# Kernel optimization log

Measured on AMD Instinct MI355X. Metric: run time of the kernel, lower is better.

The kernel has to match this reference:

```python
import jax, jax.numpy as jnp
import numpy as np

HIDDEN = 1024
NUM_HEADS = 16
HEAD_DIM = HIDDEN // NUM_HEADS  # 64
B, S = 2, 2048


def setup_inputs() -> dict:
    key = jax.random.key(0)
    ks = jax.random.split(key, 10)
    sd = 1.0 / np.sqrt(HIDDEN)
    x = jax.random.normal(ks[0], (B, S, HIDDEN), dtype=jnp.float32)
    # per-head projections stacked over head axis: [H, hidden, head_dim]
    Wq = jax.random.normal(ks[1], (NUM_HEADS, HIDDEN, HEAD_DIM), dtype=jnp.float32) * sd
    Wk = jax.random.normal(ks[2], (NUM_HEADS, HIDDEN, HEAD_DIM), dtype=jnp.float32) * sd
    Wv = jax.random.normal(ks[3], (NUM_HEADS, HIDDEN, HEAD_DIM), dtype=jnp.float32) * sd
    bq = jax.random.normal(ks[4], (NUM_HEADS, HEAD_DIM), dtype=jnp.float32) * sd
    bk = jax.random.normal(ks[5], (NUM_HEADS, HEAD_DIM), dtype=jnp.float32) * sd
    bv = jax.random.normal(ks[6], (NUM_HEADS, HEAD_DIM), dtype=jnp.float32) * sd
    # output projection: [all_head_size, hidden]
    Wo = jax.random.normal(ks[7], (HIDDEN, HIDDEN), dtype=jnp.float32) * sd
    bo = jax.random.normal(ks[8], (HIDDEN,), dtype=jnp.float32) * sd
    return {"x": x, "Wq": Wq, "bq": bq, "Wk": Wk, "bk": bk,
            "Wv": Wv, "bv": bv, "Wo": Wo, "bo": bo}


def reference(x, Wq, bq, Wk, bk, Wv, bv, Wo, bo):
    # Fused-across-heads equivalent of the per-head Python loop.
    # q,k,v: [B, H, S, Dh]
    q = jnp.einsum('bsd,hde->bhse', x, Wq) + bq[None, :, None, :]
    k = jnp.einsum('bsd,hde->bhse', x, Wk) + bk[None, :, None, :]
    v = jnp.einsum('bsd,hde->bhse', x, Wv) + bv[None, :, None, :]
    scale = 1.0 / jnp.sqrt(jnp.asarray(HEAD_DIM, dtype=x.dtype))
    scores = jnp.einsum('bhse,bhte->bhst', q, k) * scale  # [B,H,S,S]
    probs = jax.nn.softmax(scores, axis=-1)               # dropout=0 (eval)
    ctx = jnp.einsum('bhst,bhte->bhse', probs, v)         # [B,H,S,Dh]
    # concat heads on last dim (head order matches torch.cat over heads)
    ctx = jnp.transpose(ctx, (0, 2, 1, 3)).reshape(x.shape[0], x.shape[1], -1)
    out = ctx @ Wo + bo                                   # output projection
    return out
```

## Files before the change

kernel.cpp:

```cpp
#include <hip/hip_runtime.h>
#include <cstdint>

typedef unsigned short u16;
typedef __attribute__((ext_vector_type(8))) short short8;
typedef __attribute__((ext_vector_type(4))) short short4v;
typedef __attribute__((ext_vector_type(4))) float f32x4;
typedef __attribute__((ext_vector_type(4))) unsigned short u16x4;

__device__ __forceinline__ u16 f2bf(float x) {
    unsigned int u = __float_as_uint(x);
    u += 0x7fffu + ((u >> 16) & 1u);
    return (u16)(u >> 16);
}

__device__ __forceinline__ float fexp2(float x) {
#if __has_builtin(__builtin_amdgcn_exp2f)
    return __builtin_amdgcn_exp2f(x);
#else
    return exp2f(x);
#endif
}

__device__ __forceinline__ unsigned pack_bf16(float a, float b) {
    unsigned ua = __float_as_uint(a) + 0x8000u;
    unsigned ub = __float_as_uint(b) + 0x8000u;
    return __builtin_amdgcn_perm(ub, ua, 0x07060302u);
}

#if __has_builtin(__builtin_amdgcn_mfma_f32_16x16x16bf16_1k)
__device__ __forceinline__ f32x4 mfma16(short4v a, short4v b, f32x4 c) {
    return __builtin_amdgcn_mfma_f32_16x16x16bf16_1k(a, b, c, 0, 0, 0);
}
#else
__device__ __forceinline__ f32x4 mfma16(short4v a, short4v b, f32x4 c) {
    short8 a8 = {a[0], a[1], a[2], a[3], 0, 0, 0, 0};
    short8 b8 = {b[0], b[1], b[2], b[3], 0, 0, 0, 0};
    return __builtin_amdgcn_mfma_f32_16x16x32_bf16(a8, b8, c, 0, 0, 0);
}
#endif

__device__ __forceinline__ void gload_lds16(const u16* g, u16* l) {
    __builtin_amdgcn_global_load_lds(
        (const __attribute__((address_space(1))) void*)(g),
        (__attribute__((address_space(3))) void*)(l),
        16, 0, 0);
}

__global__ __launch_bounds__(256) void prep_kernel(
    const float* __restrict__ x,
    const float* __restrict__ Wq, const float* __restrict__ Wk,
    const float* __restrict__ Wv, const float* __restrict__ Wo,
    u16* __restrict__ xb, u16* __restrict__ wqkv, u16* __restrict__ wot)
{
    __shared__ u16 tile[64][65];
    const int z = blockIdx.z;
    const int tc = threadIdx.x & 63, tr = threadIdx.x >> 6;

    if (z == 1) {
        const int blk = blockIdx.y * 16 + blockIdx.x;
        const int base = (blk * 256 + threadIdx.x) * 4;
        #pragma unroll
        for (int i = 0; i < 16; ++i) {
            const int idx = base + i * 262144;
            float4 v = *(const float4*)(x + idx);
            u16x4 o;
            o.x = f2bf(v.x); o.y = f2bf(v.y); o.z = f2bf(v.z); o.w = f2bf(v.w);
            *(u16x4*)(xb + idx) = o;
        }
        return;
    }

    const float* src;
    u16* dst;
    int C, R, rb, cb;
    if (z == 0) {
        src = Wo; dst = wot; C = 1024; R = 1024;
        rb = blockIdx.x * 64; cb = blockIdx.y * 64;
    } else {
        const float* W = (z == 2) ? Wq : (z == 3) ? Wk : Wv;
        const int head = blockIdx.y;
        src = W + head * 65536;
        dst = wqkv + (size_t)(z - 2) * 1048576 + head * 65536;
        C = 64; R = 1024;
        rb = blockIdx.x * 64; cb = 0;
    }
    #pragma unroll
    for (int i = 0; i < 64; i += 4)
        tile[tr + i][tc] = f2bf(src[(size_t)(rb + tr + i) * C + (cb + tc)]);
    __syncthreads();
    #pragma unroll
    for (int i = 0; i < 64; i += 4)
        dst[(size_t)(cb + tr + i) * R + (rb + tc)] = tile[tc][tr + i];
}

__global__ __launch_bounds__(256, 3) void gemm_qkv_kernel(
    const u16* __restrict__ X, const u16* __restrict__ W,
    const float* __restrict__ bq, const float* __restrict__ bk,
    const float* __restrict__ bv,
    u16* __restrict__ qo, u16* __restrict__ ko, u16* __restrict__ vto)
{
    __shared__ __align__(16) u16 As[128 * 32];
    __shared__ __align__(16) u16 Bs[128 * 32];
    const int tid = threadIdx.x;
    const int lane = tid & 63;
    const int wv = tid >> 6;
    const int wm = wv & 1, wn = wv >> 1;
    const int m0 = blockIdx.y * 128;
    const int n0 = blockIdx.x * 128;
    const int c = lane & 15, qd = lane >> 4;

    f32x4 acc[4][4];
    #pragma unroll
    for (int a = 0; a < 4; ++a)
        #pragma unroll
        for (int b2 = 0; b2 < 4; ++b2) acc[a][b2] = f32x4{0.f, 0.f, 0.f, 0.f};

    const u16* Xb = X + (size_t)m0 * 1024;
    const u16* Wb = W + (size_t)n0 * 1024;

    for (int kt = 0; kt < 1024; kt += 32) {
        #pragma unroll
        for (int i = 0; i < 2; ++i) {
            int slot = i * 256 + tid;
            int row = slot >> 2, part = slot & 3;
            gload_lds16(Xb + (size_t)row * 1024 + kt + part * 8, &As[slot * 8]);
            gload_lds16(Wb + (size_t)row * 1024 + kt + part * 8, &Bs[slot * 8]);
        }
        __syncthreads();
        short8 af[4], bf[4];
        #pragma unroll
        for (int mt = 0; mt < 4; ++mt)
            af[mt] = *(const short8*)&As[(wm * 64 + mt * 16 + c) * 32 + qd * 8];
        #pragma unroll
        for (int nt = 0; nt < 4; ++nt)
            bf[nt] = *(const short8*)&Bs[(wn * 64 + nt * 16 + c) * 32 + qd * 8];
        #pragma unroll
        for (int mt = 0; mt < 4; ++mt)
            #pragma unroll
            for (int nt = 0; nt < 4; ++nt)
                acc[mt][nt] = __builtin_amdgcn_mfma_f32_16x16x32_bf16(af[mt], bf[nt], acc[mt][nt], 0, 0, 0);
        __syncthreads();
    }

    #pragma unroll
    for (int mt = 0; mt < 4; ++mt) {
        const int mbase = m0 + wm * 64 + mt * 16 + qd * 4;
        const int b = mbase >> 11;
        #pragma unroll
        for (int nt = 0; nt < 4; ++nt) {
            const int n = n0 + wn * 64 + nt * 16 + c;
            const int mat = n >> 10;
            const int idx = n & 1023;
            const int h = idx >> 6, e = idx & 63;
            const float bias = (mat == 0 ? bq : (mat == 1 ? bk : bv))[idx];
            if (mat == 2) {
                const int s = mbase & 2047;
                u16x4 pv;
                pv.x = f2bf(acc[mt][nt][0] + bias);
                pv.y = f2bf(acc[mt][nt][1] + bias);
                pv.z = f2bf(acc[mt][nt][2] + bias);
                pv.w = f2bf(acc[mt][nt][3] + bias);
                *(u16x4*)(vto + ((((size_t)(b * 16 + h) * 128 + (s >> 4)) * 64 + e) * 16
                                 + (s & 15))) = pv;
            } else {
                const float scale = (mat == 0) ? 0.18033688011112042f : 1.0f;
                u16* dst = (mat == 0) ? qo : ko;
                #pragma unroll
                for (int r = 0; r < 4; ++r) {
                    const int s = (mbase + r) & 2047;
                    dst[((size_t)((b * 16 + h) * 2048 + s)) * 64 + e] =
                        f2bf((acc[mt][nt][r] + bias) * scale);
                }
            }
        }
    }
}

__global__ __launch_bounds__(256, 3) void flash_kernel(
    const u16* __restrict__ Q,
    const u16* __restrict__ K,
    const u16* __restrict__ V2,
    u16* __restrict__ ctx)
{
    __shared__ __align__(16) char pool[34816];
    u16* stage = (u16*)pool;
    float (*Os)[64][66] = (float (*)[64][66])pool;
    float (*Ls)[64] = (float (*)[64])(pool + 33792);

    const int tid = threadIdx.x, lane = tid & 63, w = tid >> 6;
    const int c = lane & 15, qd = lane >> 4;
    const int bid = blockIdx.x;
    const int r5 = bid & 31;
    const int bh = (r5 & 7) * 4 + (r5 >> 3);
    const int q0 = (bid >> 5) * 64;
    const int b = bh >> 4, h = bh & 15;
    const u16* Qh = Q + (size_t)bh * 2048 * 64;
    const u16* Kh = K + (size_t)bh * 2048 * 64;
    const u16* Vh = V2 + (size_t)bh * 128 * 1024;

    u16* Kst = stage + w * 3072;

    const int krow8 = lane >> 3;
    const int kgc = (lane & 7) ^ (krow8 & 7);
    const int voff = c * 16 + qd * 4;

    short8 qf[4][2];
    #pragma unroll
    for (int qb = 0; qb < 4; ++qb)
        #pragma unroll
        for (int kb = 0; kb < 2; ++kb)
            qf[qb][kb] = *(const short8*)&Qh[(size_t)(q0 + qb * 16 + c) * 64 + kb * 32 + qd * 8];

    f32x4 o[4][4];
    float lsum[4];
    #pragma unroll
    for (int mt = 0; mt < 4; ++mt)
        #pragma unroll
        for (int qb = 0; qb < 4; ++qb) o[mt][qb] = f32x4{0.f, 0.f, 0.f, 0.f};
    #pragma unroll
    for (int qb = 0; qb < 4; ++qb) lsum[qb] = 0.f;

    #pragma unroll
    for (int j = 0; j < 2; ++j) {
        const int row = j * 8 + krow8;
        gload_lds16(Kh + (size_t)(w * 512 + row) * 64 + kgc * 8,
                    Kst + j * 512 + lane * 8);
    }
    short4v vA[4], vB[4];
    {
        const u16* vb = Vh + (size_t)(w * 32) * 1024 + voff;
        #pragma unroll
        for (int mt = 0; mt < 4; ++mt)
            vA[mt] = *(const short4v*)(vb + mt * 256);
    }
    #pragma unroll
    for (int j = 0; j < 2; ++j) {
        const int row = j * 8 + krow8;
        gload_lds16(Kh + (size_t)(w * 512 + 16 + row) * 64 + kgc * 8,
                    Kst + 1024 + j * 512 + lane * 8);
    }

    int cur = 0;
    auto body = [&](int it, short4v (&VC)[4], short4v (&VN)[4]) {
        u16* Kb = Kst + cur * 1024;

        __builtin_amdgcn_s_waitcnt(0xF74);
        __builtin_amdgcn_sched_barrier(0);

        short8 kf[2];
        #pragma unroll
        for (int kb = 0; kb < 2; ++kb)
            kf[kb] = *(const short8*)&Kb[c * 64 + ((4 * kb + qd) ^ (c & 7)) * 8];

        __builtin_amdgcn_sched_barrier(0);

        {
            const int itn = (it + 1) & 31;
            const u16* vb = Vh + (size_t)(w * 32 + itn) * 1024 + voff;
            #pragma unroll
            for (int mt = 0; mt < 4; ++mt)
                VN[mt] = *(const short4v*)(vb + mt * 256);
        }
        {
            const int itn = (it + 2) & 31;
            const int t0n = w * 512 + itn * 16;
            const int nslot = (cur >= 1) ? cur - 1 : 2;
            u16* Kn = Kst + nslot * 1024;
            #pragma unroll
            for (int j = 0; j < 2; ++j) {
                const int row = j * 8 + krow8;
                gload_lds16(Kh + (size_t)(t0n + row) * 64 + kgc * 8,
                            Kn + j * 512 + lane * 8);
            }
        }

        f32x4 sc[4];
        #pragma unroll
        for (int qb = 0; qb < 4; ++qb) {
            sc[qb] = f32x4{0.f, 0.f, 0.f, 0.f};
            sc[qb] = __builtin_amdgcn_mfma_f32_16x16x32_bf16(kf[0], qf[qb][0], sc[qb], 0, 0, 0);
            sc[qb] = __builtin_amdgcn_mfma_f32_16x16x32_bf16(kf[1], qf[qb][1], sc[qb], 0, 0, 0);
        }

        short4v pb[4];
        #pragma unroll
        for (int qb = 0; qb < 4; ++qb) {
            float p0 = fexp2(sc[qb][0]);
            float p1 = fexp2(sc[qb][1]);
            float p2 = fexp2(sc[qb][2]);
            float p3 = fexp2(sc[qb][3]);
            lsum[qb] += (p0 + p1) + (p2 + p3);
            unsigned d0 = pack_bf16(p0, p1);
            unsigned d1 = pack_bf16(p2, p3);
            union { unsigned u[2]; short4v s; } pu;
            pu.u[0] = d0; pu.u[1] = d1;
            pb[qb] = pu.s;
        }

        #pragma unroll
        for (int qb = 0; qb < 4; ++qb)
            #pragma unroll
            for (int mt = 0; mt < 4; ++mt)
                o[mt][qb] = mfma16(VC[mt], pb[qb], o[mt][qb]);

        cur = (cur == 2) ? 0 : cur + 1;
    };

    for (int it2 = 0; it2 < 16; ++it2) {
        body(2 * it2, vA, vB);
        body(2 * it2 + 1, vB, vA);
    }

    __builtin_amdgcn_s_waitcnt(0xF70);
    __syncthreads();

    #pragma unroll
    for (int qb = 0; qb < 4; ++qb) {
        lsum[qb] += __shfl_xor(lsum[qb], 16, 64);
        lsum[qb] += __shfl_xor(lsum[qb], 32, 64);
    }
    if (qd == 0) {
        #pragma unroll
        for (int qb = 0; qb < 4; ++qb) Ls[w][qb * 16 + c] = lsum[qb];
    }

    if (w >= 2) {
        float (*S)[66] = Os[w - 2];
        #pragma unroll
        for (int mt = 0; mt < 4; ++mt)
            #pragma unroll
            for (int qb = 0; qb < 4; ++qb)
                #pragma unroll
                for (int r = 0; r < 4; ++r)
                    S[mt * 16 + qd * 4 + r][qb * 16 + c] = o[mt][qb][r];
    }
    __syncthreads();
    if (w < 2) {
        float (*S)[66] = Os[w];
        #pragma unroll
        for (int mt = 0; mt < 4; ++mt)
            #pragma unroll
            for (int qb = 0; qb < 4; ++qb)
                #pragma unroll
                for (int r = 0; r < 4; ++r)
                    o[mt][qb][r] += S[mt * 16 + qd * 4 + r][qb * 16 + c];
    }
    __syncthreads();
    if (w == 1) {
        float (*S)[66] = Os[0];
        #pragma unroll
        for (int mt = 0; mt < 4; ++mt)
            #pragma unroll
            for (int qb = 0; qb < 4; ++qb)
                #pragma unroll
                for (int r = 0; r < 4; ++r)
                    S[mt * 16 + qd * 4 + r][qb * 16 + c] = o[mt][qb][r];
    }
    __syncthreads();
    if (w == 0) {
        float (*S)[66] = Os[0];
        float inv[4];
        #pragma unroll
        for (int qb = 0; qb < 4; ++qb) {
            int q = qb * 16 + c;
            float l = (Ls[0][q] + Ls[1][q]) + (Ls[2][q] + Ls[3][q]);
            inv[qb] = __builtin_amdgcn_rcpf(l);
        }
        #pragma unroll
        for (int mt = 0; mt < 4; ++mt)
            #pragma unroll
            for (int qb = 0; qb < 4; ++qb) {
                u16x4 ov;
                #pragma unroll
                for (int r = 0; r < 4; ++r) {
                    float v = (o[mt][qb][r] + S[mt * 16 + qd * 4 + r][qb * 16 + c]) * inv[qb];
                    ((u16*)&ov)[r] = f2bf(v);
                }
                *(u16x4*)&ctx[((size_t)(b * 2048 + q0 + qb * 16 + c)) * 1024
                              + h * 64 + mt * 16 + qd * 4] = ov;
            }
    }
}

__global__ __launch_bounds__(256, 4) void gemm_out_kernel(
    const u16* __restrict__ A, const u16* __restrict__ Wt,
    const float* __restrict__ bo, float* __restrict__ out)
{
    __shared__ __align__(16) u16 As[64 * 32];
    __shared__ __align__(16) u16 Bs[128 * 32];
    const int tid = threadIdx.x;
    const int lane = tid & 63;
    const int wv = tid >> 6;
    const int wm = wv & 1, wn = wv >> 1;
    const int m0 = blockIdx.x * 64;
    const int n0 = blockIdx.y * 128;
    const int c = lane & 15, qd = lane >> 4;

    f32x4 acc[2][4];
    #pragma unroll
    for (int a = 0; a < 2; ++a)
        #pragma unroll
        for (int b2 = 0; b2 < 4; ++b2) acc[a][b2] = f32x4{0.f, 0.f, 0.f, 0.f};

    const u16* Ab = A + (size_t)m0 * 1024;
    const u16* Wb = Wt + (size_t)n0 * 1024;

    for (int kt = 0; kt < 1024; kt += 32) {
        {
            int row = tid >> 2, part = tid & 3;
            gload_lds16(Ab + (size_t)row * 1024 + kt + part * 8, &As[tid * 8]);
        }
        #pragma unroll
        for (int i = 0; i < 2; ++i) {
            int slot = i * 256 + tid;
            int row = slot >> 2, part = slot & 3;
            gload_lds16(Wb + (size_t)row * 1024 + kt + part * 8, &Bs[slot * 8]);
        }
        __syncthreads();
        short8 af[2], bf[4];
        #pragma unroll
        for (int mt = 0; mt < 2; ++mt)
            af[mt] = *(const short8*)&As[(wm * 32 + mt * 16 + c) * 32 + qd * 8];
        #pragma unroll
        for (int nt = 0; nt < 4; ++nt)
            bf[nt] = *(const short8*)&Bs[(wn * 64 + nt * 16 + c) * 32 + qd * 8];
        #pragma unroll
        for (int mt = 0; mt < 2; ++mt)
            #pragma unroll
            for (int nt = 0; nt < 4; ++nt)
                acc[mt][nt] = __builtin_amdgcn_mfma_f32_16x16x32_bf16(af[mt], bf[nt], acc[mt][nt], 0, 0, 0);
        __syncthreads();
    }

    #pragma unroll
    for (int mt = 0; mt < 2; ++mt) {
        const int mbase = m0 + wm * 32 + mt * 16 + qd * 4;
        #pragma unroll
        for (int nt = 0; nt < 4; ++nt) {
            const int n = n0 + wn * 64 + nt * 16 + c;
            const float bias = bo[n];
            #pragma unroll
            for (int r = 0; r < 4; ++r)
                out[(size_t)(mbase + r) * 1024 + n] = acc[mt][nt][r] + bias;
        }
    }
}

extern "C" void kernel_launch(void* const* d_in, const int* in_sizes, int n_in,
                              void* d_out, int out_size, void* d_ws, size_t ws_size,
                              hipStream_t stream) {
    const float* x  = (const float*)d_in[0];
    const float* Wq = (const float*)d_in[1];
    const float* bq = (const float*)d_in[2];
    const float* Wk = (const float*)d_in[3];
    const float* bk = (const float*)d_in[4];
    const float* Wv = (const float*)d_in[5];
    const float* bv = (const float*)d_in[6];
    const float* Wo = (const float*)d_in[7];
    const float* bo = (const float*)d_in[8];
    float* out = (float*)d_out;

    u16* ws    = (u16*)d_ws;
    u16* xb    = ws;
    u16* wqkv  = xb + 4096 * 1024;
    u16* wot   = wqkv + 3072 * 1024;
    u16* qws   = wot + 1024 * 1024;
    u16* kws   = qws + 4194304;
    u16* v2ws  = kws + 4194304;
    u16* ctxws = v2ws + 4194304;

    prep_kernel<<<dim3(16, 16, 5), 256, 0, stream>>>(x, Wq, Wk, Wv, Wo, xb, wqkv, wot);
    gemm_qkv_kernel<<<dim3(24, 32), 256, 0, stream>>>(xb, wqkv, bq, bk, bv, qws, kws, v2ws);
    flash_kernel<<<1024, 256, 0, stream>>>(qws, kws, v2ws, ctxws);
    gemm_out_kernel<<<dim3(64, 8), 256, 0, stream>>>(ctxws, wot, bo, out);
}
```

Measured before the change: 190.7 us.

## Make flash attention kernel persistent with atomic work-queue tile scheduling

Converts the flash attention kernel into a persistent kernel launched with 768 blocks, each pulling (batch-head, query-tile) work items from a global atomic counter until all 1024 tiles are done. The goal is to cut tail imbalance and block launch overhead when the tile count is not a multiple of the resident block count. It also changes the tile ordering from the previous interleaved bh mapping to a contiguous one, which can affect L2 reuse of K/V. It adds a memset, an atomic and an extra sync per tile, and it falls back to the old launch when the workspace is too small to hold the counter.

```diff
diff --git a/kernel.cpp b/kernel.cpp
--- a/kernel.cpp
+++ b/kernel.cpp
@@ -180,23 +180,17 @@
     const u16* __restrict__ Q,
     const u16* __restrict__ K,
     const u16* __restrict__ V2,
-    u16* __restrict__ ctx)
+    u16* __restrict__ ctx,
+    unsigned* tcnt)
 {
     __shared__ __align__(16) char pool[34816];
+    __shared__ unsigned sh_t;
     u16* stage = (u16*)pool;
     float (*Os)[64][66] = (float (*)[64][66])pool;
     float (*Ls)[64] = (float (*)[64])(pool + 33792);
 
     const int tid = threadIdx.x, lane = tid & 63, w = tid >> 6;
     const int c = lane & 15, qd = lane >> 4;
-    const int bid = blockIdx.x;
-    const int r5 = bid & 31;
-    const int bh = (r5 & 7) * 4 + (r5 >> 3);
-    const int q0 = (bid >> 5) * 64;
-    const int b = bh >> 4, h = bh & 15;
-    const u16* Qh = Q + (size_t)bh * 2048 * 64;
-    const u16* Kh = K + (size_t)bh * 2048 * 64;
-    const u16* Vh = V2 + (size_t)bh * 128 * 1024;
 
     u16* Kst = stage + w * 3072;
 
@@ -204,181 +198,199 @@
     const int kgc = (lane & 7) ^ (krow8 & 7);
     const int voff = c * 16 + qd * 4;
 
-    short8 qf[4][2];
-    #pragma unroll
-    for (int qb = 0; qb < 4; ++qb)
-        #pragma unroll
-        for (int kb = 0; kb < 2; ++kb)
-            qf[qb][kb] = *(const short8*)&Qh[(size_t)(q0 + qb * 16 + c) * 64 + kb * 32 + qd * 8];
-
-    f32x4 o[4][4];
-    float lsum[4];
-    #pragma unroll
-    for (int mt = 0; mt < 4; ++mt)
-        #pragma unroll
-        for (int qb = 0; qb < 4; ++qb) o[mt][qb] = f32x4{0.f, 0.f, 0.f, 0.f};
-    #pragma unroll
-    for (int qb = 0; qb < 4; ++qb) lsum[qb] = 0.f;
-
-    #pragma unroll
-    for (int j = 0; j < 2; ++j) {
-        const int row = j * 8 + krow8;
-        gload_lds16(Kh + (size_t)(w * 512 + row) * 64 + kgc * 8,
-                    Kst + j * 512 + lane * 8);
-    }
-    short4v vA[4], vB[4];
-    {
-        const u16* vb = Vh + (size_t)(w * 32) * 1024 + voff;
+    for (;;) {
+        if (tid == 0)
+            sh_t = tcnt ? atomicAdd(tcnt, 1u) : (unsigned)blockIdx.x;
+        __syncthreads();
+        const unsigned t = sh_t;
+        if (t >= 1024u) break;
+
+        const int bh = (int)(t >> 5);
+        const int q0 = (int)(t & 31) << 6;
+        const int b = bh >> 4, h = bh & 15;
+        const u16* Qh = Q + (size_t)bh * 131072;
+        const u16* Kh = K + (size_t)bh * 131072;
+        const u16* Vh = V2 + (size_t)bh * 131072;
+
+        short8 qf[4][2];
+        #pragma unroll
+        for (int qb = 0; qb < 4; ++qb)
+            #pragma unroll
+            for (int kb = 0; kb < 2; ++kb)
+                qf[qb][kb] = *(const short8*)&Qh[(size_t)(q0 + qb * 16 + c) * 64 + kb * 32 + qd * 8];
+
+        f32x4 o[4][4];
+        float lsum[4];
         #pragma unroll
         for (int mt = 0; mt < 4; ++mt)
-            vA[mt] = *(const short4v*)(vb + mt * 256);
-    }
-    #pragma unroll
-    for (int j = 0; j < 2; ++j) {
-        const int row = j * 8 + krow8;
-        gload_lds16(Kh + (size_t)(w * 512 + 16 + row) * 64 + kgc * 8,
-                    Kst + 1024 + j * 512 + lane * 8);
-    }
-
-    int cur = 0;
-    auto body = [&](int it, short4v (&VC)[4], short4v (&VN)[4]) {
-        u16* Kb = Kst + cur * 1024;
-
-        __builtin_amdgcn_s_waitcnt(0xF74);
-        __builtin_amdgcn_sched_barrier(0);
-
-        short8 kf[2];
-        #pragma unroll
-        for (int kb = 0; kb < 2; ++kb)
-            kf[kb] = *(const short8*)&Kb[c * 64 + ((4 * kb + qd) ^ (c & 7)) * 8];
-
-        __builtin_amdgcn_sched_barrier(0);
-
+            #pragma unroll
+            for (int qb = 0; qb < 4; ++qb) o[mt][qb] = f32x4{0.f, 0.f, 0.f, 0.f};
+        #pragma unroll
+        for (int qb = 0; qb < 4; ++qb) lsum[qb] = 0.f;
+
+        #pragma unroll
+        for (int j = 0; j < 2; ++j) {
+            const int row = j * 8 + krow8;
+            gload_lds16(Kh + (size_t)(w * 512 + row) * 64 + kgc * 8,
+                        Kst + j * 512 + lane * 8);
+        }
+        short4v vA[4], vB[4];
         {
-            const int itn = (it + 1) & 31;
-            const u16* vb = Vh + (size_t)(w * 32 + itn) * 1024 + voff;
+            const u16* vb = Vh + (size_t)(w * 32) * 1024 + voff;
             #pragma unroll
             for (int mt = 0; mt < 4; ++mt)
-                VN[mt] = *(const short4v*)(vb + mt * 256);
-        }
-        {
-            const int itn = (it + 2) & 31;
-            const int t0n = w * 512 + itn * 16;
-            const int nslot = (cur >= 1) ? cur - 1 : 2;
-            u16* Kn = Kst + nslot * 1024;
-            #pragma unroll
-            for (int j = 0; j < 2; ++j) {
-                const int row = j * 8 + krow8;
-                gload_lds16(Kh + (size_t)(t0n + row) * 64 + kgc * 8,
-                            Kn + j * 512 + lane * 8);
-            }
-        }
-
-        f32x4 sc[4];
+                vA[mt] = *(const short4v*)(vb + mt * 256);
+        }
+        #pragma unroll
+        for (int j = 0; j < 2; ++j) {
+            const int row = j * 8 + krow8;
+            gload_lds16(Kh + (size_t)(w * 512 + 16 + row) * 64 + kgc * 8,
+                        Kst + 1024 + j * 512 + lane * 8);
+        }
+
+        int cur = 0;
+        auto body = [&](int it, short4v (&VC)[4], short4v (&VN)[4]) {
+            u16* Kb = Kst + cur * 1024;
+
+            __builtin_amdgcn_s_waitcnt(0xF74);
+            __builtin_amdgcn_sched_barrier(0);
+
+            short8 kf[2];
+            #pragma unroll
+            for (int kb = 0; kb < 2; ++kb)
+                kf[kb] = *(const short8*)&Kb[c * 64 + ((4 * kb + qd) ^ (c & 7)) * 8];
+
+            __builtin_amdgcn_sched_barrier(0);
+
+            {
+                const int itn = (it + 1) & 31;
+                const u16* vb = Vh + (size_t)(w * 32 + itn) * 1024 + voff;
+                #pragma unroll
+                for (int mt = 0; mt < 4; ++mt)
+                    VN[mt] = *(const short4v*)(vb + mt * 256);
+            }
+            {
+                const int itn = (it + 2) & 31;
+                const int t0n = w * 512 + itn * 16;
+                const int nslot = (cur >= 1) ? cur - 1 : 2;
+                u16* Kn = Kst + nslot * 1024;
+                #pragma unroll
+                for (int j = 0; j < 2; ++j) {
+                    const int row = j * 8 + krow8;
+                    gload_lds16(Kh + (size_t)(t0n + row) * 64 + kgc * 8,
+                                Kn + j * 512 + lane * 8);
+                }
+            }
+
+            f32x4 sc[4];
+            #pragma unroll
+            for (int qb = 0; qb < 4; ++qb) {
+                sc[qb] = f32x4{0.f, 0.f, 0.f, 0.f};
+                sc[qb] = __builtin_amdgcn_mfma_f32_16x16x32_bf16(kf[0], qf[qb][0], sc[qb], 0, 0, 0);
+                sc[qb] = __builtin_amdgcn_mfma_f32_16x16x32_bf16(kf[1], qf[qb][1], sc[qb], 0, 0, 0);
+            }
+
+            short4v pb[4];
+            #pragma unroll
+            for (int qb = 0; qb < 4; ++qb) {
+                float p0 = fexp2(sc[qb][0]);
+                float p1 = fexp2(sc[qb][1]);
+                float p2 = fexp2(sc[qb][2]);
+                float p3 = fexp2(sc[qb][3]);
+                lsum[qb] += (p0 + p1) + (p2 + p3);
+                unsigned d0 = pack_bf16(p0, p1);
+                unsigned d1 = pack_bf16(p2, p3);
+                union { unsigned u[2]; short4v s; } pu;
+                pu.u[0] = d0; pu.u[1] = d1;
+                pb[qb] = pu.s;
+            }
+
+            #pragma unroll
+            for (int qb = 0; qb < 4; ++qb)
+                #pragma unroll
+                for (int mt = 0; mt < 4; ++mt)
+                    o[mt][qb] = mfma16(VC[mt], pb[qb], o[mt][qb]);
+
+            cur = (cur == 2) ? 0 : cur + 1;
+        };
+
+        for (int it2 = 0; it2 < 16; ++it2) {
+            body(2 * it2, vA, vB);
+            body(2 * it2 + 1, vB, vA);
+        }
+
+        __builtin_amdgcn_s_waitcnt(0xF70);
+        __syncthreads();
+
         #pragma unroll
         for (int qb = 0; qb < 4; ++qb) {
-            sc[qb] = f32x4{0.f, 0.f, 0.f, 0.f};
-            sc[qb] = __builtin_amdgcn_mfma_f32_16x16x32_bf16(kf[0], qf[qb][0], sc[qb], 0, 0, 0);
-            sc[qb] = __builtin_amdgcn_mfma_f32_16x16x32_bf16(kf[1], qf[qb][1], sc[qb], 0, 0, 0);
-        }
-
-        short4v pb[4];
-        #pragma unroll
-        for (int qb = 0; qb < 4; ++qb) {
-            float p0 = fexp2(sc[qb][0]);
-            float p1 = fexp2(sc[qb][1]);
-            float p2 = fexp2(sc[qb][2]);
-            float p3 = fexp2(sc[qb][3]);
-            lsum[qb] += (p0 + p1) + (p2 + p3);
-            unsigned d0 = pack_bf16(p0, p1);
-            unsigned d1 = pack_bf16(p2, p3);
-            union { unsigned u[2]; short4v s; } pu;
-            pu.u[0] = d0; pu.u[1] = d1;
-            pb[qb] = pu.s;
-        }
-
-        #pragma unroll
-        for (int qb = 0; qb < 4; ++qb)
+            lsum[qb] += __shfl_xor(lsum[qb], 16, 64);
+            lsum[qb] += __shfl_xor(lsum[qb], 32, 64);
+        }
+        if (qd == 0) {
+            #pragma unroll
+            for (int qb = 0; qb < 4; ++qb) Ls[w][qb * 16 + c] = lsum[qb];
+        }
+
+        if (w >= 2) {
+            float (*S)[66] = Os[w - 2];
             #pragma unroll
             for (int mt = 0; mt < 4; ++mt)
-                o[mt][qb] = mfma16(VC[mt], pb[qb], o[mt][qb]);
-
-        cur = (cur == 2) ? 0 : cur + 1;
-    };
-
-    for (int it2 = 0; it2 < 16; ++it2) {
-        body(2 * it2, vA, vB);
-        body(2 * it2 + 1, vB, vA);
-    }
-
-    __builtin_amdgcn_s_waitcnt(0xF70);
-    __syncthreads();
-
-    #pragma unroll
-    for (int qb = 0; qb < 4; ++qb) {
-        lsum[qb] += __shfl_xor(lsum[qb], 16, 64);
-        lsum[qb] += __shfl_xor(lsum[qb], 32, 64);
-    }
-    if (qd == 0) {
-        #pragma unroll
-        for (int qb = 0; qb < 4; ++qb) Ls[w][qb * 16 + c] = lsum[qb];
-    }
-
-    if (w >= 2) {
-        float (*S)[66] = Os[w - 2];
-        #pragma unroll
-        for (int mt = 0; mt < 4; ++mt)
-            #pragma unroll
-            for (int qb = 0; qb < 4; ++qb)
-                #pragma unroll
-                for (int r = 0; r < 4; ++r)
-                    S[mt * 16 + qd * 4 + r][qb * 16 + c] = o[mt][qb][r];
-    }
-    __syncthreads();
-    if (w < 2) {
-        float (*S)[66] = Os[w];
-        #pragma unroll
-        for (int mt = 0; mt < 4; ++mt)
-            #pragma unroll
-            for (int qb = 0; qb < 4; ++qb)
-                #pragma unroll
-                for (int r = 0; r < 4; ++r)
-                    o[mt][qb][r] += S[mt * 16 + qd * 4 + r][qb * 16 + c];
-    }
-    __syncthreads();
-    if (w == 1) {
-        float (*S)[66] = Os[0];
-        #pragma unroll
-        for (int mt = 0; mt < 4; ++mt)
-            #pragma unroll
-            for (int qb = 0; qb < 4; ++qb)
-                #pragma unroll
-                for (int r = 0; r < 4; ++r)
-                    S[mt * 16 + qd * 4 + r][qb * 16 + c] = o[mt][qb][r];
-    }
-    __syncthreads();
-    if (w == 0) {
-        float (*S)[66] = Os[0];
-        float inv[4];
-        #pragma unroll
-        for (int qb = 0; qb < 4; ++qb) {
-            int q = qb * 16 + c;
-            float l = (Ls[0][q] + Ls[1][q]) + (Ls[2][q] + Ls[3][q]);
-            inv[qb] = __builtin_amdgcn_rcpf(l);
-        }
-        #pragma unroll
-        for (int mt = 0; mt < 4; ++mt)
+                #pragma unroll
+                for (int qb = 0; qb < 4; ++qb)
+                    #pragma unroll
+                    for (int r = 0; r < 4; ++r)
+                        S[mt * 16 + qd * 4 + r][qb * 16 + c] = o[mt][qb][r];
+        }
+        __syncthreads();
+        if (w < 2) {
+            float (*S)[66] = Os[w];
+            #pragma unroll
+            for (int mt = 0; mt < 4; ++mt)
+                #pragma unroll
+                for (int qb = 0; qb < 4; ++qb)
+                    #pragma unroll
+                    for (int r = 0; r < 4; ++r)
+                        o[mt][qb][r] += S[mt * 16 + qd * 4 + r][qb * 16 + c];
+        }
+        __syncthreads();
+        if (w == 1) {
+            float (*S)[66] = Os[0];
+            #pragma unroll
+            for (int mt = 0; mt < 4; ++mt)
+                #pragma unroll
+                for (int qb = 0; qb < 4; ++qb)
+                    #pragma unroll
+                    for (int r = 0; r < 4; ++r)
+                        S[mt * 16 + qd * 4 + r][qb * 16 + c] = o[mt][qb][r];
+        }
+        __syncthreads();
+        if (w == 0) {
+            float (*S)[66] = Os[0];
+            float inv[4];
             #pragma unroll
             for (int qb = 0; qb < 4; ++qb) {
-                u16x4 ov;
-                #pragma unroll
-                for (int r = 0; r < 4; ++r) {
-                    float v = (o[mt][qb][r] + S[mt * 16 + qd * 4 + r][qb * 16 + c]) * inv[qb];
-                    ((u16*)&ov)[r] = f2bf(v);
+                int q = qb * 16 + c;
+                float l = (Ls[0][q] + Ls[1][q]) + (Ls[2][q] + Ls[3][q]);
+                inv[qb] = __builtin_amdgcn_rcpf(l);
+            }
+            #pragma unroll
+            for (int mt = 0; mt < 4; ++mt)
+                #pragma unroll
+                for (int qb = 0; qb < 4; ++qb) {
+                    u16x4 ov;
+                    #pragma unroll
+                    for (int r = 0; r < 4; ++r) {
+                        float v = (o[mt][qb][r] + S[mt * 16 + qd * 4 + r][qb * 16 + c]) * inv[qb];
+                        ((u16*)&ov)[r] = f2bf(v);
+                    }
+                    *(u16x4*)&ctx[((size_t)(b * 2048 + q0 + qb * 16 + c)) * 1024
+                                  + h * 64 + mt * 16 + qd * 4] = ov;
                 }
-                *(u16x4*)&ctx[((size_t)(b * 2048 + q0 + qb * 16 + c)) * 1024
-                              + h * 64 + mt * 16 + qd * 4] = ov;
-            }
+        }
+
+        __syncthreads();
+        if (!tcnt) break;
     }
 }
 
@@ -468,9 +480,17 @@
     u16* kws   = qws + 4194304;
     u16* v2ws  = kws + 4194304;
     u16* ctxws = v2ws + 4194304;
+    const size_t cnt_off = 50331648;
+    unsigned* tcnt = (ws_size >= cnt_off + 64)
+                   ? (unsigned*)((char*)d_ws + cnt_off) : nullptr;
 
     prep_kernel<<<dim3(16, 16, 5), 256, 0, stream>>>(x, Wq, Wk, Wv, Wo, xb, wqkv, wot);
     gemm_qkv_kernel<<<dim3(24, 32), 256, 0, stream>>>(xb, wqkv, bq, bk, bv, qws, kws, v2ws);
-    flash_kernel<<<1024, 256, 0, stream>>>(qws, kws, v2ws, ctxws);
+    if (tcnt) {
+        hipMemsetAsync(tcnt, 0, 4, stream);
+        flash_kernel<<<768, 256, 0, stream>>>(qws, kws, v2ws, ctxws, tcnt);
+    } else {
+        flash_kernel<<<1024, 256, 0, stream>>>(qws, kws, v2ws, ctxws, nullptr);
+    }
     gemm_out_kernel<<<dim3(64, 8), 256, 0, stream>>>(ctxws, wot, bo, out);
 }
```

Result: slower. 214.8 us (+12.6%).

## Restructure QKV GEMM with 256x256 tiles, double-buffered async LDS loads and swizzle

Applied to the files above, without the earlier changes.

The QKV projection GEMM moves from 128x128 tiles with 4 waves to 256x256 tiles with 8 waves. LDS is double-buffered, so global-to-LDS loads for the next two k-steps overlap with the MFMA work, using explicit waitcnt and barriers. It also adds an XOR swizzle on LDS columns to avoid bank conflicts and remaps block IDs for L2 locality. Larger tiles raise data reuse but cut the grid to 192 blocks and raise register pressure, which may leave some CUs underused.

```diff
diff --git a/kernel.cpp b/kernel.cpp
--- a/kernel.cpp
+++ b/kernel.cpp
@@ -93,62 +93,94 @@
         dst[(size_t)(cb + tr + i) * R + (rb + tc)] = tile[tc][tr + i];
 }
 
-__global__ __launch_bounds__(256, 3) void gemm_qkv_kernel(
+__global__ __launch_bounds__(512, 2) void gemm_qkv_kernel(
     const u16* __restrict__ X, const u16* __restrict__ W,
     const float* __restrict__ bq, const float* __restrict__ bk,
     const float* __restrict__ bv,
     u16* __restrict__ qo, u16* __restrict__ ko, u16* __restrict__ vto)
 {
-    __shared__ __align__(16) u16 As[128 * 32];
-    __shared__ __align__(16) u16 Bs[128 * 32];
+    __shared__ __align__(16) u16 lds[32768];
     const int tid = threadIdx.x;
     const int lane = tid & 63;
-    const int wv = tid >> 6;
-    const int wm = wv & 1, wn = wv >> 1;
-    const int m0 = blockIdx.y * 128;
-    const int n0 = blockIdx.x * 128;
+    const int wid = tid >> 6;
+    const int wm = wid >> 2;
+    const int wn = wid & 3;
     const int c = lane & 15, qd = lane >> 4;
 
-    f32x4 acc[4][4];
-    #pragma unroll
-    for (int a = 0; a < 4; ++a)
-        #pragma unroll
-        for (int b2 = 0; b2 < 4; ++b2) acc[a][b2] = f32x4{0.f, 0.f, 0.f, 0.f};
+    const int id = (blockIdx.x & 7) * 24 + (blockIdx.x >> 3);
+    const int m0 = (id / 12) * 256;
+    const int n0 = (id % 12) * 256;
 
     const u16* Xb = X + (size_t)m0 * 1024;
     const u16* Wb = W + (size_t)n0 * 1024;
 
-    for (int kt = 0; kt < 1024; kt += 32) {
-        #pragma unroll
-        for (int i = 0; i < 2; ++i) {
-            int slot = i * 256 + tid;
-            int row = slot >> 2, part = slot & 3;
-            gload_lds16(Xb + (size_t)row * 1024 + kt + part * 8, &As[slot * 8]);
-            gload_lds16(Wb + (size_t)row * 1024 + kt + part * 8, &Bs[slot * 8]);
-        }
-        __syncthreads();
-        short8 af[4], bf[4];
-        #pragma unroll
-        for (int mt = 0; mt < 4; ++mt)
-            af[mt] = *(const short8*)&As[(wm * 64 + mt * 16 + c) * 32 + qd * 8];
-        #pragma unroll
-        for (int nt = 0; nt < 4; ++nt)
-            bf[nt] = *(const short8*)&Bs[(wn * 64 + nt * 16 + c) * 32 + qd * 8];
-        #pragma unroll
-        for (int mt = 0; mt < 4; ++mt)
-            #pragma unroll
-            for (int nt = 0; nt < 4; ++nt)
-                acc[mt][nt] = __builtin_amdgcn_mfma_f32_16x16x32_bf16(af[mt], bf[nt], acc[mt][nt], 0, 0, 0);
-        __syncthreads();
-    }
-
-    #pragma unroll
-    for (int mt = 0; mt < 4; ++mt) {
-        const int mbase = m0 + wm * 64 + mt * 16 + qd * 4;
+    const int srow = tid >> 2;
+    const int scg  = (lane & 3) ^ ((lane >> 3) & 3);
+    const int cof = (qd ^ ((c >> 1) & 3)) * 8;
+    const int rA0 = wm * 128 + c;
+    const int rB0 = wn * 64 + c;
+
+    auto stage = [&](int t, int p) {
+        const int pb = p * 16384;
+        #pragma unroll
+        for (int j = 0; j < 2; ++j) {
+            const int row = j * 128 + srow;
+            const u16* gs = Xb + (size_t)row * 1024 + t * 32 + scg * 8;
+            gload_lds16(gs, &lds[pb + (j * 512 + tid) * 8]);
+            const u16* gw = Wb + (size_t)row * 1024 + t * 32 + scg * 8;
+            gload_lds16(gw, &lds[pb + 8192 + (j * 512 + tid) * 8]);
+        }
+    };
+
+    f32x4 acc[8][4];
+    #pragma unroll
+    for (int mi = 0; mi < 8; ++mi)
+        #pragma unroll
+        for (int ni = 0; ni < 4; ++ni) acc[mi][ni] = f32x4{0.f, 0.f, 0.f, 0.f};
+
+    auto body = [&](int t) {
+        const int pb = (t & 1) * 16384;
+        __builtin_amdgcn_sched_barrier(0);
+        __builtin_amdgcn_s_barrier();
+        __builtin_amdgcn_sched_barrier(0);
+        short8 af[8], bf[4];
+        #pragma unroll
+        for (int mi = 0; mi < 8; ++mi)
+            af[mi] = *(const short8*)&lds[pb + (rA0 + mi * 16) * 32 + cof];
+        #pragma unroll
+        for (int ni = 0; ni < 4; ++ni)
+            bf[ni] = *(const short8*)&lds[pb + 8192 + (rB0 + ni * 16) * 32 + cof];
+        __builtin_amdgcn_s_setprio(1);
+        #pragma unroll
+        for (int mi = 0; mi < 8; ++mi)
+            #pragma unroll
+            for (int ni = 0; ni < 4; ++ni)
+                acc[mi][ni] = __builtin_amdgcn_mfma_f32_16x16x32_bf16(af[mi], bf[ni], acc[mi][ni], 0, 0, 0);
+        __builtin_amdgcn_s_setprio(0);
+        __builtin_amdgcn_sched_barrier(0);
+        __builtin_amdgcn_s_barrier();
+    };
+
+    stage(0, 0);
+    stage(1, 1);
+    __builtin_amdgcn_sched_barrier(0);
+
+    for (int t = 0; t < 31; ++t) {
+        __builtin_amdgcn_s_waitcnt(0xF74);
+        body(t);
+        if (t < 30) stage(t + 2, t & 1);
+        __builtin_amdgcn_sched_barrier(0);
+    }
+    __builtin_amdgcn_s_waitcnt(0xF70);
+    body(31);
+
+    #pragma unroll
+    for (int mi = 0; mi < 8; ++mi) {
+        const int mbase = m0 + wm * 128 + mi * 16 + qd * 4;
         const int b = mbase >> 11;
         #pragma unroll
-        for (int nt = 0; nt < 4; ++nt) {
-            const int n = n0 + wn * 64 + nt * 16 + c;
+        for (int ni = 0; ni < 4; ++ni) {
+            const int n = n0 + wn * 64 + ni * 16 + c;
             const int mat = n >> 10;
             const int idx = n & 1023;
             const int h = idx >> 6, e = idx & 63;
@@ -156,10 +188,10 @@
             if (mat == 2) {
                 const int s = mbase & 2047;
                 u16x4 pv;
-                pv.x = f2bf(acc[mt][nt][0] + bias);
-                pv.y = f2bf(acc[mt][nt][1] + bias);
-                pv.z = f2bf(acc[mt][nt][2] + bias);
-                pv.w = f2bf(acc[mt][nt][3] + bias);
+                pv.x = f2bf(acc[mi][ni][0] + bias);
+                pv.y = f2bf(acc[mi][ni][1] + bias);
+                pv.z = f2bf(acc[mi][ni][2] + bias);
+                pv.w = f2bf(acc[mi][ni][3] + bias);
                 *(u16x4*)(vto + ((((size_t)(b * 16 + h) * 128 + (s >> 4)) * 64 + e) * 16
                                  + (s & 15))) = pv;
             } else {
@@ -169,7 +201,7 @@
                 for (int r = 0; r < 4; ++r) {
                     const int s = (mbase + r) & 2047;
                     dst[((size_t)((b * 16 + h) * 2048 + s)) * 64 + e] =
-                        f2bf((acc[mt][nt][r] + bias) * scale);
+                        f2bf((acc[mi][ni][r] + bias) * scale);
                 }
             }
         }
@@ -470,7 +502,7 @@
     u16* ctxws = v2ws + 4194304;
 
     prep_kernel<<<dim3(16, 16, 5), 256, 0, stream>>>(x, Wq, Wk, Wv, Wo, xb, wqkv, wot);
-    gemm_qkv_kernel<<<dim3(24, 32), 256, 0, stream>>>(xb, wqkv, bq, bk, bv, qws, kws, v2ws);
+    gemm_qkv_kernel<<<192, 512, 0, stream>>>(xb, wqkv, bq, bk, bv, qws, kws, v2ws);
     flash_kernel<<<1024, 256, 0, stream>>>(qws, kws, v2ws, ctxws);
     gemm_out_kernel<<<dim3(64, 8), 256, 0, stream>>>(ctxws, wot, bo, out);
 }
```

New measurement: 195.0 us. 2.2% more time.
